# Optimization experiments

Hardware: AMD Instinct MI355X
Metric: run time of the kernel (lower is better)

The kernel has to match this reference:

```python
import jax, jax.numpy as jnp
import numpy as np

D = 256
H = 8
DH = D // H
N = 100000
B = 256
T = 131072
HID_FUSE = 256   # fuse MLP hidden = d_model
HID_HEAD = 256   # QuantileHeads hidden
NQ = 3           # quantiles (q10, q50, q90)


def setup_inputs() -> dict:
    key = jax.random.key(0)
    ks = jax.random.split(key, 32)
    p = lambda k, *s: (0.02 * jax.random.normal(k, s, dtype=jnp.float32))
    inp = {
        'node_embeddings': jax.random.normal(ks[0], (N, D), dtype=jnp.float32),
        'target_index': jax.random.randint(ks[1], (B,), 0, N),
        'port_index': jax.random.randint(ks[2], (T,), 0, N),
        'port_batch': jnp.sort(jax.random.randint(ks[3], (T,), 0, B)),
        'port_weight': jax.random.uniform(ks[4], (T,), dtype=jnp.float32),
        # PMA pooling params (learnable seed + MHA projections, no biases)
        'seed': p(ks[5], D),
        'Wq_p': p(ks[6], D, D), 'Wk_p': p(ks[7], D, D), 'Wv_p': p(ks[8], D, D), 'Wo_p': p(ks[9], D, D),
        # target->portfolio cross-attention params
        'Wq_c': p(ks[10], D, D), 'Wk_c': p(ks[11], D, D), 'Wv_c': p(ks[12], D, D), 'Wo_c': p(ks[13], D, D),
        # fuse LayerNorm(3d) + MLP
        'ln_g': jnp.ones((3 * D,), jnp.float32), 'ln_b': jnp.zeros((3 * D,), jnp.float32),
        'fuse_W1': p(ks[14], 3 * D, HID_FUSE), 'fuse_b1': jnp.zeros((HID_FUSE,), jnp.float32),
        'fuse_W2': p(ks[15], HID_FUSE, D), 'fuse_b2': jnp.zeros((D,), jnp.float32),
        # quantile heads MLP
        'head_W1': p(ks[16], D, HID_HEAD), 'head_b1': jnp.zeros((HID_HEAD,), jnp.float32),
        'head_W2': p(ks[17], HID_HEAD, NQ), 'head_b2': jnp.zeros((NQ,), jnp.float32),
    }
    return inp


def _segment_attend(logits, v, seg, num_segments):
    # logits [T,H], v [T,H,DH], seg [T] -> pooled [num_segments, H, DH]
    m = jax.ops.segment_max(logits, seg, num_segments=num_segments)  # [B,H]
    e = jnp.exp(logits - m[seg])                                      # [T,H]
    s = jax.ops.segment_sum(e, seg, num_segments=num_segments)        # [B,H]
    p = e / (s[seg] + 1e-9)
    return jax.ops.segment_sum(p[..., None] * v, seg, num_segments=num_segments)


def reference(node_embeddings, target_index, port_index, port_batch, port_weight,
              seed, Wq_p, Wk_p, Wv_p, Wo_p, Wq_c, Wk_c, Wv_c, Wo_c,
              ln_g, ln_b, fuse_W1, fuse_b1, fuse_W2, fuse_b2,
              head_W1, head_b1, head_W2, head_b2):
    b = target_index.shape[0]
    scale = float(DH) ** -0.5
    tgt = node_embeddings[target_index]          # [B,D]
    tok = node_embeddings[port_index]            # [T,D]
    logw = jnp.log(port_weight + 1e-8)           # DV01 weighting as logit bias

    # --- PMA: learnable seed query pools DV01-weighted portfolio tokens ---
    q_p = (seed @ Wq_p).reshape(H, DH)
    k_p = (tok @ Wk_p).reshape(-1, H, DH)
    v_p = (tok @ Wv_p).reshape(-1, H, DH)
    lg_p = jnp.einsum('thd,hd->th', k_p, q_p) * scale + logw[:, None]
    pooled = _segment_attend(lg_p, v_p, port_batch, b).reshape(b, D)
    contexts = pooled @ Wo_p                     # [B,D]; zeros for empty portfolios

    # --- target -> portfolio cross-attention (residual) ---
    q_c = (tgt @ Wq_c).reshape(b, H, DH)
    k_c = (tok @ Wk_c).reshape(-1, H, DH)
    v_c = (tok @ Wv_c).reshape(-1, H, DH)
    lg_c = jnp.einsum('thd,thd->th', k_c, q_c[port_batch]) * scale + logw[:, None]
    att = _segment_attend(lg_c, v_c, port_batch, b).reshape(b, D)
    fused = tgt + att @ Wo_c                     # [B,D]; == tgt for empty portfolios

    # --- fuse: concat -> LN -> MLP ---
    z = jnp.concatenate([tgt, contexts, fused], axis=-1)  # [B,3D]
    mu = jnp.mean(z, axis=-1, keepdims=True)
    var = jnp.var(z, axis=-1, keepdims=True)
    z = (z - mu) * jax.lax.rsqrt(var + 1e-5) * ln_g + ln_b
    z = jax.nn.relu(z @ fuse_W1 + fuse_b1) @ fuse_W2 + fuse_b2  # [B,D]

    # --- quantile heads ---
    out = jax.nn.relu(z @ head_W1 + head_b1) @ head_W2 + head_b2  # [B,NQ]
    return out
```

## Files before the change

kernel.cpp:

```cpp
#include <hip/hip_runtime.h>
#include <hip/hip_bf16.h>

typedef __attribute__((ext_vector_type(8))) short short8;
typedef __attribute__((ext_vector_type(4))) float floatx4;

#define SCALE 0.17677669529663687f

__device__ __forceinline__ unsigned short f2bf(float f) {
  unsigned int x = __float_as_uint(f);
  x += 0x7fffu + ((x >> 16) & 1u);
  return (unsigned short)(x >> 16);
}
__device__ __forceinline__ float bf2f(unsigned short u) {
  return __uint_as_float(((unsigned int)u) << 16);
}

__device__ __forceinline__ short8 load_cvt8(const float* p) {
  floatx4 a = *(const floatx4*)p;
  floatx4 b = *(const floatx4*)(p + 4);
  short8 r;
  r[0] = (short)f2bf(a[0]); r[1] = (short)f2bf(a[1]);
  r[2] = (short)f2bf(a[2]); r[3] = (short)f2bf(a[3]);
  r[4] = (short)f2bf(b[0]); r[5] = (short)f2bf(b[1]);
  r[6] = (short)f2bf(b[2]); r[7] = (short)f2bf(b[3]);
  return r;
}

__device__ __forceinline__ void matvec256(const float* __restrict__ W,
                                          const float* act, float* outv,
                                          float* red4, int tid) {
  const int c4 = tid & 63, kg = tid >> 6, c0 = c4 * 4;
  floatx4 acc = (floatx4){0.f, 0.f, 0.f, 0.f};
  const float* Wp = W + (size_t)(kg * 64) * 256 + c0;
  const float* ap = act + kg * 64;
  #pragma unroll 8
  for (int k = 0; k < 64; ++k) {
    floatx4 wv = *(const floatx4*)(Wp + (size_t)k * 256);
    float a = ap[k];
    acc[0] += a * wv[0]; acc[1] += a * wv[1];
    acc[2] += a * wv[2]; acc[3] += a * wv[3];
  }
  *(floatx4*)(red4 + kg * 256 + c0) = acc;
  __syncthreads();
  outv[tid] = red4[tid] + red4[256 + tid] + red4[512 + tid] + red4[768 + tid];
  __syncthreads();
}

__global__ __launch_bounds__(256) void setup_kernel(
    const float* __restrict__ node,
    const int* __restrict__ tgt_idx,
    const int* __restrict__ port_batch,
    const float* __restrict__ seed,
    const float* __restrict__ Wq_p,
    const float* __restrict__ Wk_p,
    const float* __restrict__ Wq_c,
    const float* __restrict__ Wk_c,
    unsigned short* __restrict__ u_p_t,
    unsigned short* __restrict__ u_c_all,
    int* __restrict__ seg, int T, int B)
{
  __shared__ float act_l[256];
  __shared__ float q_l[256];
  __shared__ __align__(16) float red4[1024];
  const int tid = threadIdx.x;
  const int b = blockIdx.x;

  if (tid == 0 || (tid == 64 && b == B - 1)) {
    int key = (tid == 0) ? b : B;
    int lo = 0, hi = T;
    while (lo < hi) { int mid = (lo + hi) >> 1; if (port_batch[mid] < key) lo = mid + 1; else hi = mid; }
    seg[key] = lo;
  }

  act_l[tid] = node[(size_t)tgt_idx[b] * 256 + tid];
  __syncthreads();
  matvec256(Wq_c, act_l, q_l, red4, tid);

  {
    float hs[8];
    #pragma unroll
    for (int h = 0; h < 8; ++h) hs[h] = 0.f;
    #pragma unroll
    for (int c = 0; c < 32; ++c) {
      floatx4 wa = *(const floatx4*)(Wk_c + (size_t)tid * 256 + c * 8);
      floatx4 wb = *(const floatx4*)(Wk_c + (size_t)tid * 256 + c * 8 + 4);
      const int h = c >> 2;
      #pragma unroll
      for (int j = 0; j < 4; ++j) hs[h] += wa[j] * q_l[c * 8 + j];
      #pragma unroll
      for (int j = 0; j < 4; ++j) hs[h] += wb[j] * q_l[c * 8 + 4 + j];
    }
    #pragma unroll
    for (int h = 0; h < 8; ++h)
      u_c_all[(size_t)b * 2048 + h * 256 + tid] = f2bf(hs[h]);
  }

  if (b == 0) {
    __syncthreads();
    act_l[tid] = seed[tid];
    __syncthreads();
    matvec256(Wq_p, act_l, q_l, red4, tid);
    float hs[8];
    #pragma unroll
    for (int h = 0; h < 8; ++h) hs[h] = 0.f;
    #pragma unroll
    for (int c = 0; c < 32; ++c) {
      floatx4 wa = *(const floatx4*)(Wk_p + (size_t)tid * 256 + c * 8);
      floatx4 wb = *(const floatx4*)(Wk_p + (size_t)tid * 256 + c * 8 + 4);
      const int h = c >> 2;
      #pragma unroll
      for (int j = 0; j < 4; ++j) hs[h] += wa[j] * q_l[c * 8 + j];
      #pragma unroll
      for (int j = 0; j < 4; ++j) hs[h] += wb[j] * q_l[c * 8 + 4 + j];
    }
    #pragma unroll
    for (int h = 0; h < 8; ++h) u_p_t[h * 256 + tid] = f2bf(hs[h]);
  }
}

__global__ __launch_bounds__(256, 2) void attn_kernel(
    const float* __restrict__ node,
    const int* __restrict__ port_index,
    const float* __restrict__ port_weight,
    const unsigned short* __restrict__ u_p_t,
    const unsigned short* __restrict__ u_c_all,
    const int* __restrict__ seg,
    float* __restrict__ slabs, int T, int S)
{
  __shared__ __align__(16) unsigned short tok_lds[64 * 264];
  __shared__ __align__(16) unsigned short E_t[16 * 72];
  __shared__ float l_lds[16];

  const int tid  = threadIdx.x;
  const int s    = blockIdx.x;
  const int b    = blockIdx.y;
  const int lane = tid & 63;
  const int w    = tid >> 6;
  const int q    = lane >> 4;
  const int n    = lane & 15;

  if (tid < 16) l_lds[tid] = 0.f;

  short8 ufrag[8];
  const unsigned short* ubase = (n < 8) ? (u_p_t + n * 256)
                                        : (u_c_all + (size_t)b * 2048 + (n - 8) * 256);
  #pragma unroll
  for (int s8 = 0; s8 < 8; ++s8)
    ufrag[s8] = *(const short8*)(ubase + q * 8 + s8 * 32);

  const int start  = seg[b];
  const int end    = seg[b + 1];
  const int ntiles = (end - start + 63) >> 6;

  floatx4 sacc[4];
  #pragma unroll
  for (int nt = 0; nt < 4; ++nt) sacc[nt] = (floatx4){0.f, 0.f, 0.f, 0.f};

  __syncthreads();

  for (int it = s; it < ntiles; it += S) {
    const int tbase = start + it * 64;
    short8 cur[8];
    {
      int t = tbase + w * 16 + n; int tc = t < T ? t : T - 1;
      const float* rp = node + (size_t)port_index[tc] * 256 + q * 8;
      #pragma unroll
      for (int k = 0; k < 8; ++k) cur[k] = load_cvt8(rp + k * 32);
    }
    float pw[4];
    #pragma unroll
    for (int r = 0; r < 4; ++r) { int tr = tbase + w * 16 + q * 4 + r; pw[r] = port_weight[tr < T ? tr : T - 1]; }

    floatx4 lacc = (floatx4){0.f, 0.f, 0.f, 0.f};
    #pragma unroll
    for (int k = 0; k < 8; ++k)
      lacc = __builtin_amdgcn_mfma_f32_16x16x32_bf16(cur[k], ufrag[k], lacc, 0, 0, 0);
    float lsum = 0.f;
    #pragma unroll
    for (int r = 0; r < 4; ++r) {
      const int tr = tbase + w * 16 + q * 4 + r;
      float e = 0.f;
      if (tr < end) {
        float lg = lacc[r] * SCALE + logf(pw[r] + 1e-8f);
        e = __expf(lg);
      }
      unsigned short eb = f2bf(e);
      E_t[n * 72 + w * 16 + q * 4 + r] = eb;
      lsum += bf2f(eb);
    }
    lsum += __shfl_xor(lsum, 16, 64);
    lsum += __shfl_xor(lsum, 32, 64);
    if (lane < 16) atomicAdd(&l_lds[lane], lsum);
    #pragma unroll
    for (int k = 0; k < 8; ++k)
      *(short8*)(tok_lds + (w * 16 + n) * 264 + q * 8 + k * 32) = cur[k];
    __syncthreads();
    short8 ea0 = *(const short8*)(E_t + n * 72 + q * 8);
    short8 ea1 = *(const short8*)(E_t + n * 72 + 32 + q * 8);
    #pragma unroll
    for (int nt = 0; nt < 4; ++nt) {
      const int dcol = w * 64 + nt * 16 + n;
      short8 b0, b1;
      #pragma unroll
      for (int j = 0; j < 8; ++j) b0[j] = (short)tok_lds[(q * 8 + j) * 264 + dcol];
      #pragma unroll
      for (int j = 0; j < 8; ++j) b1[j] = (short)tok_lds[(32 + q * 8 + j) * 264 + dcol];
      sacc[nt] = __builtin_amdgcn_mfma_f32_16x16x32_bf16(ea0, b0, sacc[nt], 0, 0, 0);
      sacc[nt] = __builtin_amdgcn_mfma_f32_16x16x32_bf16(ea1, b1, sacc[nt], 0, 0, 0);
    }
    __syncthreads();
  }

  float* stage = (float*)tok_lds;
  #pragma unroll
  for (int nt = 0; nt < 4; ++nt)
    #pragma unroll
    for (int r = 0; r < 4; ++r)
      stage[(q * 4 + r) * 256 + w * 64 + nt * 16 + n] = sacc[nt][r];
  __syncthreads();
  float* sl = slabs + ((size_t)b * S + s) * 4224;
  #pragma unroll
  for (int i = 0; i < 4; ++i) {
    const int row = i * 4 + w;
    const int c0 = (tid & 63) * 4;
    *(floatx4*)(sl + row * 256 + c0) = *(const floatx4*)(stage + row * 256 + c0);
  }
  if (tid < 16) sl[4096 + tid] = l_lds[tid];
}

__global__ __launch_bounds__(256) void k_slab_gemm(
    const float* __restrict__ slabs, int S,
    const float* __restrict__ Wv_p, const float* __restrict__ Wv_c,
    float* __restrict__ X)
{
  __shared__ float act_l[4 * 256];
  __shared__ float lsum[4];
  const int tid = threadIdx.x;
  const int bt = blockIdx.x, nt = blockIdx.y, z = blockIdx.z;
  const int head = nt >> 1;
  const int row = z * 8 + head;
  if (tid < 4) {
    const float* sl = slabs + (size_t)(bt * 4 + tid) * S * 4224;
    float l = 0.f;
    for (int s = 0; s < S; ++s) l += sl[s * 4224 + 4096 + row];
    lsum[tid] = 1.0f / (l + 1e-9f);
  }
  __syncthreads();
  for (int i = tid; i < 4 * 256; i += 256) {
    int m = i >> 8, k = i & 255;
    const float* sl = slabs + (size_t)(bt * 4 + m) * S * 4224;
    float sum = 0.f;
    for (int s = 0; s < S; ++s) sum += sl[s * 4224 + row * 256 + k];
    act_l[i] = sum * lsum[m];
  }
  __syncthreads();
  const int m = tid >> 6, lane = tid & 63, ks = lane >> 4, n = lane & 15;
  const int n0 = nt * 16;
  const float* W = z ? Wv_c : Wv_p;
  float acc = 0.f;
  const float* Wp = W + (size_t)(ks * 64) * 256 + n0 + n;
  const float* ap = &act_l[m * 256 + ks * 64];
  #pragma unroll 8
  for (int k = 0; k < 64; ++k) acc += ap[k] * Wp[(size_t)k * 256];
  acc += __shfl_xor(acc, 16, 64);
  acc += __shfl_xor(acc, 32, 64);
  if (ks == 0)
    X[(size_t)(bt * 4 + m) * 512 + z * 256 + n0 + n] = acc;
}

__global__ __launch_bounds__(256) void k_plain_gemm(
    const float* __restrict__ act, int act_ld,
    const float* __restrict__ W0, const float* __restrict__ W1,
    const float* __restrict__ bias0, const float* __restrict__ bias1,
    float* __restrict__ outp, int out_ld,
    int K, int relu)
{
  __shared__ float act_l[4 * 768];
  const int tid = threadIdx.x;
  const int bt = blockIdx.x, nt = blockIdx.y, z = blockIdx.z;
  const float* W = z ? W1 : W0;
  const float* bias = z ? bias1 : bias0;
  for (int i = tid; i < 4 * K; i += 256) {
    int m = i / K, k = i - m * K;
    act_l[m * K + k] = act[(size_t)(bt * 4 + m) * act_ld + z * K + k];
  }
  __syncthreads();
  const int m = tid >> 6, lane = tid & 63, ks = lane >> 4, n = lane & 15;
  const int n0 = nt * 16;
  const int Kq = K >> 2;
  float acc = 0.f;
  const float* Wp = W + (size_t)(ks * Kq) * 256 + n0 + n;
  const float* ap = &act_l[m * K + ks * Kq];
  #pragma unroll 8
  for (int k = 0; k < Kq; ++k) acc += ap[k] * Wp[(size_t)k * 256];
  acc += __shfl_xor(acc, 16, 64);
  acc += __shfl_xor(acc, 32, 64);
  if (ks == 0) {
    float v = acc + (bias ? bias[n0 + n] : 0.f);
    if (relu) v = fmaxf(v, 0.f);
    outp[(size_t)(bt * 4 + m) * out_ld + z * 256 + n0 + n] = v;
  }
}

__global__ __launch_bounds__(256) void k_ln_gemm(
    const float* __restrict__ node, const int* __restrict__ tgt_idx,
    const float* __restrict__ zbuf,
    const float* __restrict__ ln_g, const float* __restrict__ ln_b,
    const float* __restrict__ fuse_W1, const float* __restrict__ fuse_b1,
    float* __restrict__ h1)
{
  __shared__ float act_l[4 * 768];
  const int tid = threadIdx.x;
  const int bt = blockIdx.x, nt = blockIdx.y;
  for (int i = tid; i < 4 * 256; i += 256) {
    int m = i >> 8, k = i & 255;
    int b = bt * 4 + m;
    float tg = node[(size_t)tgt_idx[b] * 256 + k];
    float C  = zbuf[(size_t)b * 512 + k];
    float Fp = zbuf[(size_t)b * 512 + 256 + k];
    act_l[m * 768 + k]       = tg;
    act_l[m * 768 + 256 + k] = C;
    act_l[m * 768 + 512 + k] = tg + Fp;
  }
  __syncthreads();
  const int m = tid >> 6, lane = tid & 63;
  {
    float s = 0.f;
    for (int k = lane; k < 768; k += 64) s += act_l[m * 768 + k];
    #pragma unroll
    for (int o = 32; o >= 1; o >>= 1) s += __shfl_xor(s, o, 64);
    const float mu = s * (1.0f / 768.0f);
    float v = 0.f;
    for (int k = lane; k < 768; k += 64) { float d = act_l[m * 768 + k] - mu; v += d * d; }
    #pragma unroll
    for (int o = 32; o >= 1; o >>= 1) v += __shfl_xor(v, o, 64);
    const float rstd = 1.0f / sqrtf(v * (1.0f / 768.0f) + 1e-5f);
    for (int k = lane; k < 768; k += 64)
      act_l[m * 768 + k] = (act_l[m * 768 + k] - mu) * rstd * ln_g[k] + ln_b[k];
  }
  __syncthreads();
  const int ks = lane >> 4, n = lane & 15;
  const int n0 = nt * 16;
  float acc = 0.f;
  const float* Wp = fuse_W1 + (size_t)(ks * 192) * 256 + n0 + n;
  const float* ap = &act_l[m * 768 + ks * 192];
  #pragma unroll 8
  for (int k = 0; k < 192; ++k) acc += ap[k] * Wp[(size_t)k * 256];
  acc += __shfl_xor(acc, 16, 64);
  acc += __shfl_xor(acc, 32, 64);
  if (ks == 0)
    h1[(size_t)(bt * 4 + m) * 256 + n0 + n] = fmaxf(acc + fuse_b1[n0 + n], 0.f);
}

__global__ __launch_bounds__(256) void k_outhead(
    const float* __restrict__ hh, const float* __restrict__ head_W2,
    const float* __restrict__ head_b2, float* __restrict__ out)
{
  const int tid = threadIdx.x;
  const int m = tid >> 6, lane = tid & 63;
  const int b = blockIdx.x * 4 + m;
  float a0 = 0.f, a1 = 0.f, a2 = 0.f;
  for (int k = lane; k < 256; k += 64) {
    float h = hh[(size_t)b * 256 + k];
    a0 += h * head_W2[k * 3 + 0];
    a1 += h * head_W2[k * 3 + 1];
    a2 += h * head_W2[k * 3 + 2];
  }
  #pragma unroll
  for (int o = 32; o >= 1; o >>= 1) {
    a0 += __shfl_xor(a0, o, 64);
    a1 += __shfl_xor(a1, o, 64);
    a2 += __shfl_xor(a2, o, 64);
  }
  if (lane == 0) {
    out[b * 3 + 0] = a0 + head_b2[0];
    out[b * 3 + 1] = a1 + head_b2[1];
    out[b * 3 + 2] = a2 + head_b2[2];
  }
}

extern "C" void kernel_launch(void* const* d_in, const int* in_sizes, int n_in,
                              void* d_out, int out_size, void* d_ws, size_t ws_size,
                              hipStream_t stream) {
  const float* node        = (const float*)d_in[0];
  const int*   tgt_idx     = (const int*)d_in[1];
  const int*   port_index  = (const int*)d_in[2];
  const int*   port_batch  = (const int*)d_in[3];
  const float* port_weight = (const float*)d_in[4];
  const float* seed        = (const float*)d_in[5];
  const float* Wq_p = (const float*)d_in[6];
  const float* Wk_p = (const float*)d_in[7];
  const float* Wv_p = (const float*)d_in[8];
  const float* Wo_p = (const float*)d_in[9];
  const float* Wq_c = (const float*)d_in[10];
  const float* Wk_c = (const float*)d_in[11];
  const float* Wv_c = (const float*)d_in[12];
  const float* Wo_c = (const float*)d_in[13];
  const float* ln_g = (const float*)d_in[14];
  const float* ln_b = (const float*)d_in[15];
  const float* fuse_W1 = (const float*)d_in[16];
  const float* fuse_b1 = (const float*)d_in[17];
  const float* fuse_W2 = (const float*)d_in[18];
  const float* fuse_b2 = (const float*)d_in[19];
  const float* head_W1 = (const float*)d_in[20];
  const float* head_b1 = (const float*)d_in[21];
  const float* head_W2 = (const float*)d_in[22];
  const float* head_b2 = (const float*)d_in[23];

  const int B = in_sizes[1];
  const int T = in_sizes[2];

  char* ws = (char*)d_ws;
  unsigned short* u_p_t   = (unsigned short*)ws;
  int*            seg     = (int*)(ws + 4096);
  unsigned short* u_c_all = (unsigned short*)(ws + 8192);
  float* X    = (float*)(ws + 8192);
  float* zbuf = (float*)(ws + 8192 + (size_t)B * 2048);
  size_t slab_off = 8192 + (size_t)B * 4096;
  float* slabs = (float*)(ws + slab_off);
  float* h1 = slabs;
  float* z2 = h1 + (size_t)B * 256;
  float* hh = z2 + (size_t)B * 256;

  size_t per_slice = (size_t)B * 4224 * 4;
  int S = 1;
  if (ws_size > slab_off) {
    size_t fit = (ws_size - slab_off) / per_slice;
    S = (int)(fit < 1 ? 1 : (fit > 4 ? 4 : fit));
  }

  const int BT = B / 4;

  setup_kernel<<<B, 256, 0, stream>>>(node, tgt_idx, port_batch, seed,
      Wq_p, Wk_p, Wq_c, Wk_c, u_p_t, u_c_all, seg, T, B);
  attn_kernel<<<dim3(S, B), 256, 0, stream>>>(node, port_index, port_weight,
      u_p_t, u_c_all, seg, slabs, T, S);
  k_slab_gemm<<<dim3(BT, 16, 2), 256, 0, stream>>>(slabs, S, Wv_p, Wv_c, X);
  k_plain_gemm<<<dim3(BT, 16, 2), 256, 0, stream>>>(X, 512, Wo_p, Wo_c,
      nullptr, nullptr, zbuf, 512, 256, 0);
  k_ln_gemm<<<dim3(BT, 16), 256, 0, stream>>>(node, tgt_idx, zbuf,
      ln_g, ln_b, fuse_W1, fuse_b1, h1);
  k_plain_gemm<<<dim3(BT, 16, 1), 256, 0, stream>>>(h1, 256, fuse_W2, nullptr,
      fuse_b2, nullptr, z2, 256, 256, 0);
  k_plain_gemm<<<dim3(BT, 16, 1), 256, 0, stream>>>(z2, 256, head_W1, nullptr,
      head_b1, nullptr, hh, 256, 256, 1);
  k_outhead<<<BT, 256, 0, stream>>>(hh, head_W2, head_b2, (float*)d_out);
}
```

Measured before the change: 319.6 us.

## Split setup into batched Q-projection and K-fold kernels; raise slab split cap

Replaces the per-target setup kernel, which ran one 256-thread block per target doing serial matvecs with block-wide reductions, with two grid-parallel kernels. The first computes the Q projections for four targets per block plus the seed row. The second folds Q through Wk into per-head bf16 vectors and performs the segment-boundary binary searches. The attention split count S may now rise from 4 to 8 when workspace allows, with an extra q_all buffer carved from the workspace. This adds a kernel launch and an intermediate round-trip through global memory in exchange for more parallelism in setup and in attention.

```diff
diff --git a/kernel.cpp b/kernel.cpp
--- a/kernel.cpp
+++ b/kernel.cpp
@@ -26,95 +26,76 @@
   return r;
 }
 
-__device__ __forceinline__ void matvec256(const float* __restrict__ W,
-                                          const float* act, float* outv,
-                                          float* red4, int tid) {
-  const int c4 = tid & 63, kg = tid >> 6, c0 = c4 * 4;
-  floatx4 acc = (floatx4){0.f, 0.f, 0.f, 0.f};
-  const float* Wp = W + (size_t)(kg * 64) * 256 + c0;
-  const float* ap = act + kg * 64;
+__global__ __launch_bounds__(256) void k_qc_gemm(
+    const float* __restrict__ node, const int* __restrict__ tgt_idx,
+    const float* __restrict__ seed,
+    const float* __restrict__ Wq_c, const float* __restrict__ Wq_p,
+    float* __restrict__ q_all, int B)
+{
+  __shared__ float act_l[4 * 256];
+  const int tid = threadIdx.x;
+  const int bt = blockIdx.x, nt = blockIdx.y;
+  const int BT = B >> 2;
+  for (int i = tid; i < 4 * 256; i += 256) {
+    int m = i >> 8, k = i & 255;
+    int b = bt * 4 + m;
+    float v = 0.f;
+    if (b < B)       v = node[(size_t)tgt_idx[b] * 256 + k];
+    else if (b == B) v = seed[k];
+    act_l[i] = v;
+  }
+  __syncthreads();
+  const float* W = (bt == BT) ? Wq_p : Wq_c;
+  const int m = tid >> 6, lane = tid & 63, ks = lane >> 4, n = lane & 15;
+  const int n0 = nt * 16;
+  float acc = 0.f;
+  const float* Wp = W + (size_t)(ks * 64) * 256 + n0 + n;
+  const float* ap = &act_l[m * 256 + ks * 64];
   #pragma unroll 8
-  for (int k = 0; k < 64; ++k) {
-    floatx4 wv = *(const floatx4*)(Wp + (size_t)k * 256);
-    float a = ap[k];
-    acc[0] += a * wv[0]; acc[1] += a * wv[1];
-    acc[2] += a * wv[2]; acc[3] += a * wv[3];
-  }
-  *(floatx4*)(red4 + kg * 256 + c0) = acc;
-  __syncthreads();
-  outv[tid] = red4[tid] + red4[256 + tid] + red4[512 + tid] + red4[768 + tid];
-  __syncthreads();
-}
-
-__global__ __launch_bounds__(256) void setup_kernel(
-    const float* __restrict__ node,
-    const int* __restrict__ tgt_idx,
-    const int* __restrict__ port_batch,
-    const float* __restrict__ seed,
-    const float* __restrict__ Wq_p,
-    const float* __restrict__ Wk_p,
-    const float* __restrict__ Wq_c,
-    const float* __restrict__ Wk_c,
-    unsigned short* __restrict__ u_p_t,
-    unsigned short* __restrict__ u_c_all,
+  for (int k = 0; k < 64; ++k) acc += ap[k] * Wp[(size_t)k * 256];
+  acc += __shfl_xor(acc, 16, 64);
+  acc += __shfl_xor(acc, 32, 64);
+  const int b = bt * 4 + m;
+  if (ks == 0 && b <= B) q_all[(size_t)b * 256 + n0 + n] = acc;
+}
+
+__global__ __launch_bounds__(256) void k_fold(
+    const float* __restrict__ Wk_c, const float* __restrict__ Wk_p,
+    const float* __restrict__ q_all, const int* __restrict__ port_batch,
+    unsigned short* __restrict__ u_c_all, unsigned short* __restrict__ u_p_t,
     int* __restrict__ seg, int T, int B)
 {
-  __shared__ float act_l[256];
-  __shared__ float q_l[256];
-  __shared__ __align__(16) float red4[1024];
-  const int tid = threadIdx.x;
-  const int b = blockIdx.x;
-
-  if (tid == 0 || (tid == 64 && b == B - 1)) {
-    int key = (tid == 0) ? b : B;
-    int lo = 0, hi = T;
-    while (lo < hi) { int mid = (lo + hi) >> 1; if (port_batch[mid] < key) lo = mid + 1; else hi = mid; }
-    seg[key] = lo;
-  }
-
-  act_l[tid] = node[(size_t)tgt_idx[b] * 256 + tid];
-  __syncthreads();
-  matvec256(Wq_c, act_l, q_l, red4, tid);
-
-  {
-    float hs[8];
-    #pragma unroll
-    for (int h = 0; h < 8; ++h) hs[h] = 0.f;
-    #pragma unroll
-    for (int c = 0; c < 32; ++c) {
-      floatx4 wa = *(const floatx4*)(Wk_c + (size_t)tid * 256 + c * 8);
-      floatx4 wb = *(const floatx4*)(Wk_c + (size_t)tid * 256 + c * 8 + 4);
-      const int h = c >> 2;
-      #pragma unroll
-      for (int j = 0; j < 4; ++j) hs[h] += wa[j] * q_l[c * 8 + j];
-      #pragma unroll
-      for (int j = 0; j < 4; ++j) hs[h] += wb[j] * q_l[c * 8 + 4 + j];
+  const int tid = threadIdx.x;
+  const int bt = blockIdx.x, dt = blockIdx.y;
+  const int BT = B >> 2;
+  if (dt == 0) {
+    int key = -1;
+    if (bt < BT) { if (tid < 4) key = bt * 4 + tid; }
+    else if (tid == 0) key = B;
+    if (key >= 0) {
+      int lo = 0, hi = T;
+      while (lo < hi) { int mid = (lo + hi) >> 1; if (port_batch[mid] < key) lo = mid + 1; else hi = mid; }
+      seg[key] = lo;
     }
-    #pragma unroll
-    for (int h = 0; h < 8; ++h)
-      u_c_all[(size_t)b * 2048 + h * 256 + tid] = f2bf(hs[h]);
-  }
-
-  if (b == 0) {
-    __syncthreads();
-    act_l[tid] = seed[tid];
-    __syncthreads();
-    matvec256(Wq_p, act_l, q_l, red4, tid);
-    float hs[8];
-    #pragma unroll
-    for (int h = 0; h < 8; ++h) hs[h] = 0.f;
-    #pragma unroll
-    for (int c = 0; c < 32; ++c) {
-      floatx4 wa = *(const floatx4*)(Wk_p + (size_t)tid * 256 + c * 8);
-      floatx4 wb = *(const floatx4*)(Wk_p + (size_t)tid * 256 + c * 8 + 4);
-      const int h = c >> 2;
-      #pragma unroll
-      for (int j = 0; j < 4; ++j) hs[h] += wa[j] * q_l[c * 8 + j];
-      #pragma unroll
-      for (int j = 0; j < 4; ++j) hs[h] += wb[j] * q_l[c * 8 + 4 + j];
-    }
-    #pragma unroll
-    for (int h = 0; h < 8; ++h) u_p_t[h * 256 + tid] = f2bf(hs[h]);
+  }
+  const int m = tid >> 6, lane = tid & 63;
+  const int b = bt * 4 + m;
+  if (b > B) return;
+  const float* Wk = (b == B) ? Wk_p : Wk_c;
+  const float* q = q_all + (size_t)b * 256;
+  #pragma unroll
+  for (int t2 = 0; t2 < 2; ++t2) {
+    const int idx = t2 * 64 + lane;
+    const int h = idx >> 4;
+    const int d = dt * 16 + (idx & 15);
+    float acc = 0.f;
+    const float* wr = Wk + (size_t)d * 256 + h * 32;
+    const float* qr = q + h * 32;
+    #pragma unroll 8
+    for (int j = 0; j < 32; ++j) acc += wr[j] * qr[j];
+    unsigned short v = f2bf(acc);
+    if (b < B) u_c_all[(size_t)b * 2048 + h * 256 + d] = v;
+    else       u_p_t[h * 256 + d] = v;
   }
 }
 
@@ -423,16 +404,22 @@
   float* hh = z2 + (size_t)B * 256;
 
   size_t per_slice = (size_t)B * 4224 * 4;
+  size_t q_off = slab_off + 8 * per_slice;
+  float* q_all = (float*)(ws + q_off);
+
   int S = 1;
-  if (ws_size > slab_off) {
-    size_t fit = (ws_size - slab_off) / per_slice;
-    S = (int)(fit < 1 ? 1 : (fit > 4 ? 4 : fit));
-  }
+  if (ws_size > slab_off + per_slice) {
+    size_t fit = (ws_size - slab_off - ((size_t)(B + 1) * 1024 + 4096)) / per_slice;
+    S = (int)(fit < 1 ? 1 : (fit > 8 ? 8 : fit));
+  }
+  if (S < 8) q_all = (float*)(ws + slab_off + (size_t)S * per_slice);
 
   const int BT = B / 4;
 
-  setup_kernel<<<B, 256, 0, stream>>>(node, tgt_idx, port_batch, seed,
-      Wq_p, Wk_p, Wq_c, Wk_c, u_p_t, u_c_all, seg, T, B);
+  k_qc_gemm<<<dim3(BT + 1, 16), 256, 0, stream>>>(node, tgt_idx, seed,
+      Wq_c, Wq_p, q_all, B);
+  k_fold<<<dim3(BT + 1, 16), 256, 0, stream>>>(Wk_c, Wk_p, q_all, port_batch,
+      u_c_all, u_p_t, seg, T, B);
   attn_kernel<<<dim3(S, B), 256, 0, stream>>>(node, port_index, port_weight,
       u_p_t, u_c_all, seg, slabs, T, S);
   k_slab_gemm<<<dim3(BT, 16, 2), 256, 0, stream>>>(slabs, S, Wv_p, Wv_c, X);
```

Result: no change. 320.7 us (+0.3%).
